# Kernel tuning notes

Hardware: AMD Instinct MI355X
Metric: run time of the kernel (lower is better)

Reference implementation:

```python
import jax, jax.numpy as jnp
import numpy as np

DN = ('NCHW', 'OIHW', 'NCHW')

def conv(x, w, b=None, pad='SAME'):
    y = jax.lax.conv_general_dilated(x, w, (1, 1), pad, dimension_numbers=DN)
    if b is not None:
        y = y + b[None, :, None, None]
    return y

def prelu(x, a):
    return jnp.where(x >= 0, x, a * x)

def ca_layer(x, w_a, w_b):
    # global avg pool -> 1x1 conv -> relu -> 1x1 conv -> sigmoid -> gate
    g = jnp.mean(x, axis=(2, 3), keepdims=True)          # [B,C,1,1]
    g = jax.nn.relu(conv(g, w_a))
    g = jax.nn.sigmoid(conv(g, w_b))
    return x * g

def head(x, w, b, ca_a, ca_b):
    y = conv(x, w, b)                                    # [B,4,H,W]
    y = ca_layer(y, ca_a, ca_b)
    return jax.nn.softmax(y, axis=1)                     # Softmax2d = softmax over C

def box_kernel(k):
    return jnp.full((1, 1, k, k), 1.0 / (k * k), dtype=jnp.float32)

def multiscale_blur(x):
    # SAME-padded uniform box filters of sizes 1,5,15,25 on [B,1,H,W]
    return [x if k == 1 else conv(x, box_kernel(k)) for k in (1, 5, 15, 25)]

def weighted_combine(h, blurs):
    # h: [B,4,H,W] softmax weights; blurs: list of 4 [B,1,H,W]
    return sum(h[:, i:i+1] * blurs[i] for i in range(4))

def setup_inputs() -> dict:
    key = jax.random.key(0)
    ks = jax.random.split(key, 32)
    B, H, W = 8, 512, 512
    s = 0.05
    inp = {
        'x':  jax.random.normal(ks[0], (B, 1, H, W), jnp.float32),
        'w1': jax.random.normal(ks[1], (32, 1, 3, 3), jnp.float32) * s,
        'b1': jnp.zeros((32,), jnp.float32),
        'a1': jnp.float32(0.25),
        'w2': jax.random.normal(ks[2], (64, 32, 3, 3), jnp.float32) * s,
        'b2': jnp.zeros((64,), jnp.float32),
        'a2': jnp.float32(0.25),
        'w3': jax.random.normal(ks[3], (32, 64, 3, 3), jnp.float32) * s,
        'b3': jnp.zeros((32,), jnp.float32),
        'a3': jnp.float32(0.25),
    }
    for i, kk in zip((1, 2, 3), (4, 8, 12)):
        inp[f'hw{i}'] = jax.random.normal(ks[kk], (4, 32, 3, 3), jnp.float32) * s
        inp[f'hb{i}'] = jnp.zeros((4,), jnp.float32)
        inp[f'ca{i}a'] = jax.random.normal(ks[kk + 1], (4, 4, 1, 1), jnp.float32) * s
        inp[f'ca{i}b'] = jax.random.normal(ks[kk + 2], (4, 4, 1, 1), jnp.float32) * s
    return inp

def reference(x, w1, b1, a1, w2, b2, a2, w3, b3, a3,
              hw1, hb1, ca1a, ca1b, hw2, hb2, ca2a, ca2b, hw3, hb3, ca3a, ca3b):
    body = prelu(conv(x, w1, b1), a1)
    body = prelu(conv(body, w2, b2), a2)
    body = prelu(conv(body, w3, b3), a3)            # [B,32,H,W]
    h1 = head(body, hw1, hb1, ca1a, ca1b)
    h2 = head(body, hw2, hb2, ca2a, ca2b)
    h3 = head(body, hw3, hb3, ca3a, ca3b)
    out1 = weighted_combine(h1, multiscale_blur(x))
    out2 = weighted_combine(h2, multiscale_blur(out1))
    out3 = weighted_combine(h3, multiscale_blur(out2))
    return out3
```

## Files before the change

kernel.cpp:

```cpp
#include <hip/hip_runtime.h>

#define HH 512
#define WW 512
#define NB 8
#define HWSZ (HH * WW)
#define PW 516
#define PROWS 514

typedef float f32x4 __attribute__((ext_vector_type(4)));
typedef float f32x16 __attribute__((ext_vector_type(16)));
typedef short bf16x8 __attribute__((ext_vector_type(8)));

__device__ __forceinline__ unsigned short f2bf(float f) {
  union { float f; unsigned u; } v; v.f = f;
  unsigned r = v.u + 0x7FFFu + ((v.u >> 16) & 1u);
  return (unsigned short)(r >> 16);
}
__device__ __forceinline__ float bf2f(unsigned u16) {
  union { unsigned u; float f; } v; v.u = u16 << 16;
  return v.f;
}

__device__ __forceinline__ void gload16(const uint4* g, uint4* l) {
  __builtin_amdgcn_global_load_lds((__attribute__((address_space(1))) void*)g,
                                   (__attribute__((address_space(3))) void*)l, 16, 0, 0);
}

#define PS1 ((size_t)PROWS * PW * 32)
#define PS2 ((size_t)PROWS * PW * 64)
#define NZ1 (2 * 4 * PW * 8 + 512 * 4 * 16)
#define NZ2 (2 * 8 * PW * 8 + 512 * 8 * 16)

__device__ __forceinline__ void zp(unsigned short* buf, int NCH, int i) {
  int rowShorts = NCH * PW * 8;
  if (i < 2 * rowShorts) {
    size_t r = (i < rowShorts) ? 0 : 513;
    int j = i % rowShorts;
    buf[r * rowShorts + j] = 0;
    return;
  }
  i -= 2 * rowShorts;
  int perRow = NCH * 16;
  int r = 1 + i / perRow;
  int j = i % perRow;
  int ch = j >> 4;
  int c = (j & 8) ? 513 : 0;
  int e = j & 7;
  buf[(((size_t)r * NCH + ch) * PW + c) * 8 + e] = 0;
}

__global__ __launch_bounds__(256) void k_prep(const float* __restrict__ w2,
                                              const float* __restrict__ w3,
                                              const float* __restrict__ h0,
                                              const float* __restrict__ h1,
                                              const float* __restrict__ h2,
                                              unsigned short* __restrict__ wp2,
                                              unsigned short* __restrict__ wp3,
                                              unsigned short* __restrict__ wph,
                                              unsigned short* __restrict__ t1,
                                              unsigned short* __restrict__ t2,
                                              float* __restrict__ S) {
  int i = blockIdx.x * 256 + threadIdx.x;
  const int N1 = 9 * 64 * 32;
  const int N2 = N1 + 9 * 32 * 64;
  const int N3 = N2 + 9 * 16 * 32;
  const int N4 = N3 + 4 * NZ1;
  const int N5 = N4 + 4 * NZ2;
  const int N6 = N5 + 128;
  if (i < N1) {
    int ic = i & 31, t = i >> 5, oc = t & 63, k = t >> 6;
    wp2[i] = f2bf(w2[(oc * 32 + ic) * 9 + k]);
  } else if (i < N2) {
    int j = i - N1;
    int ic = j & 63, t = j >> 6, oc = t & 31, k = t >> 5;
    wp3[j] = f2bf(w3[(oc * 64 + ic) * 9 + k]);
  } else if (i < N3) {
    int j = i - N2;
    int ic = j & 31, t = j >> 5, oc = t & 15, k = t >> 4;
    float v = 0.f;
    if (oc < 12) {
      const float* w = oc < 4 ? h0 : (oc < 8 ? h1 : h2);
      v = w[((oc & 3) * 32 + ic) * 9 + k];
    }
    wph[j] = f2bf(v);
  } else if (i < N4) {
    int j = i - N3;
    zp(t1 + (size_t)(j / NZ1) * PS1, 4, j % NZ1);
  } else if (i < N5) {
    int j = i - N4;
    zp(t2 + (size_t)(j / NZ2) * PS2, 8, j % NZ2);
  } else if (i < N6) {
    S[i - N5] = 0.f;
  }
}

__global__ __launch_bounds__(256) void k_conv1(const float* __restrict__ x,
                                               const float* __restrict__ w,
                                               const float* __restrict__ bias,
                                               const float* __restrict__ a_ptr,
                                               unsigned short* __restrict__ out) {
  const float* xp = x + (size_t)blockIdx.z * HWSZ;
  uint4* out4 = (uint4*)(out + (size_t)blockIdx.z * PS1);
  int pix = blockIdx.x * 256 + threadIdx.x;
  int h = pix >> 9, wc = pix & 511;
  float t[9];
#pragma unroll
  for (int dh = 0; dh < 3; dh++)
#pragma unroll
    for (int dw = 0; dw < 3; dw++) {
      int hh = h + dh - 1, ww = wc + dw - 1;
      t[dh * 3 + dw] =
          (hh >= 0 && hh < HH && ww >= 0 && ww < WW) ? xp[hh * WW + ww] : 0.f;
    }
  float a = a_ptr[0];
  unsigned pk[16];
#pragma unroll
  for (int oc = 0; oc < 32; oc++) {
    float s = bias[oc];
#pragma unroll
    for (int k = 0; k < 9; k++) s = fmaf(w[oc * 9 + k], t[k], s);
    s = s >= 0.f ? s : a * s;
    unsigned short b = f2bf(s);
    if (oc & 1)
      pk[oc >> 1] |= ((unsigned)b) << 16;
    else
      pk[oc >> 1] = b;
  }
#pragma unroll
  for (int q = 0; q < 4; q++)
    out4[((size_t)(h + 1) * 4 + q) * PW + (wc + 1)] = *(uint4*)&pk[q * 4];
}

__global__ __launch_bounds__(256, 2) void k_convm2(const unsigned short* __restrict__ in,
                                                   const unsigned short* __restrict__ wp,
                                                   const float* __restrict__ bias,
                                                   const float* __restrict__ a_ptr,
                                                   unsigned short* __restrict__ out) {
  __shared__ __align__(16) short ring[10 * 4 * 68 * 8];
  __shared__ __align__(16) short wlds[9 * 64 * 32];
  const int tid = threadIdx.x, lane = tid & 63, wid = tid >> 6;
  const int l31 = lane & 31, h16 = lane >> 5;
  const int c0 = blockIdx.x * 64;
  const int R0 = blockIdx.y * 32;
  const uint4* in4 = (const uint4*)(in + (size_t)blockIdx.z * PS1);
  unsigned short* outz = out + (size_t)blockIdx.z * PS2;
  uint4* ring4 = (uint4*)ring;
  uint4* wl4 = (uint4*)wlds;

  for (int c = tid; c < 9 * 64 * 4; c += 256) {
    int q = c & 3;
    int oc = (c >> 2) & 63;
    uint4 v = *(const uint4*)(wp + (size_t)(c >> 2) * 32 + q * 8);
    wl4[(c & ~3) | (q ^ (oc & 3))] = v;
  }

  auto load_rows = [&](int rfirst, int nrows) {
    int nseg = nrows * 4;
    for (int sg = wid; sg < nseg; sg += 4) {
      int rr = rfirst + (sg >> 2);
      int ch = sg & 3;
      const uint4* src = in4 + (size_t)(rr * 4 + ch) * PW + c0;
      uint4* dst = ring4 + ((rr % 10) * 4 + ch) * 68;
      gload16(src + lane, dst);
      gload16(src + 4 + lane, dst + 4);
    }
  };

  const float alpha = a_ptr[0];
  load_rows(R0, 6);

  for (int k = 0; k < 8; ++k) {
    const int rb = R0 + 4 * k;
    __syncthreads();
    if (k < 7) load_rows(rb + 6, 4);

    f32x16 acc[2][2];
#pragma unroll
    for (int nt = 0; nt < 2; nt++)
#pragma unroll
      for (int mt = 0; mt < 2; mt++)
#pragma unroll
        for (int j = 0; j < 16; j++) acc[nt][mt][j] = 0.f;

#pragma unroll
    for (int dh = 0; dh < 3; dh++) {
      bf16x8 af[3][2][2];
#pragma unroll
      for (int dw = 0; dw < 3; dw++)
#pragma unroll
        for (int ks = 0; ks < 2; ks++)
#pragma unroll
          for (int mt = 0; mt < 2; mt++)
            af[dw][ks][mt] = *(const bf16x8*)(
                wlds + ((((dh * 3 + dw) * 64 + mt * 32 + l31) * 4 +
                         ((ks * 2 + h16) ^ (l31 & 3))) * 8));
      const short* lrow = ring + (size_t)(((rb + wid + dh) % 10) * 4) * 68 * 8;
#pragma unroll
      for (int dw = 0; dw < 3; dw++) {
        const int pl0 = l31 + dw, pl1 = 32 + l31 + dw;
#pragma unroll
        for (int ks = 0; ks < 2; ks++) {
          const int blk = ks * 2 + h16;
          bf16x8 b0 = *(const bf16x8*)(lrow + (blk * 68 + pl0) * 8);
          bf16x8 b1 = *(const bf16x8*)(lrow + (blk * 68 + pl1) * 8);
#pragma unroll
          for (int mt = 0; mt < 2; mt++)
            acc[0][mt] = __builtin_amdgcn_mfma_f32_32x32x16_bf16(af[dw][ks][mt],
                                                                 b0, acc[0][mt], 0, 0, 0);
#pragma unroll
          for (int mt = 0; mt < 2; mt++)
            acc[1][mt] = __builtin_amdgcn_mfma_f32_32x32x16_bf16(af[dw][ks][mt],
                                                                 b1, acc[1][mt], 0, 0, 0);
        }
      }
    }

    const int orow = rb + wid + 1;
    uint2* o2 = (uint2*)outz;
#pragma unroll
    for (int nt = 0; nt < 2; nt++) {
      const int ocol = c0 + nt * 32 + l31 + 1;
#pragma unroll
      for (int mt = 0; mt < 2; mt++)
#pragma unroll
        for (int g = 0; g < 4; g++) {
          int oc0 = mt * 32 + g * 8 + h16 * 4;
          f32x4 bv = *(const f32x4*)(bias + oc0);
          float v[4];
#pragma unroll
          for (int j = 0; j < 4; j++) {
            float s = acc[nt][mt][g * 4 + j] + bv[j];
            v[j] = s >= 0.f ? s : alpha * s;
          }
          uint2 pk;
          pk.x = (unsigned)f2bf(v[0]) | ((unsigned)f2bf(v[1]) << 16);
          pk.y = (unsigned)f2bf(v[2]) | ((unsigned)f2bf(v[3]) << 16);
          size_t idx16 = ((size_t)orow * 8 + (mt * 4 + g)) * PW + ocol;
          o2[idx16 * 2 + h16] = pk;
        }
    }
  }
}

__global__ __launch_bounds__(256, 2) void k_convm3(const unsigned short* __restrict__ in,
                                                   const unsigned short* __restrict__ wp,
                                                   const float* __restrict__ bias,
                                                   const float* __restrict__ a_ptr,
                                                   unsigned short* __restrict__ out) {
  __shared__ __align__(16) short lds[8 * 8 * 68 * 8];
  const int tid = threadIdx.x, lane = tid & 63, wid = tid >> 6;
  const int l31 = lane & 31, h16 = lane >> 5;
  const int c0 = blockIdx.x * 64;
  const int R0 = blockIdx.y * 32;
  const uint4* in4 = (const uint4*)(in + (size_t)blockIdx.z * PS2);
  unsigned short* outz = out + (size_t)blockIdx.z * PS1;
  uint4* lds4 = (uint4*)lds;

  bf16x8 af[9][4];
#pragma unroll
  for (int k9 = 0; k9 < 9; k9++)
#pragma unroll
    for (int ks = 0; ks < 4; ks++)
      af[k9][ks] = *(const bf16x8*)(
          wp + ((size_t)(k9 * 32 + l31) * 64 + ks * 16 + h16 * 8));

  auto load_rows = [&](int rfirst, int nrows) {
    int nseg = nrows * 8;
    for (int sg = wid; sg < nseg; sg += 4) {
      int rr = rfirst + (sg >> 3);
      int ch = sg & 7;
      const uint4* src = in4 + (size_t)(rr * 8 + ch) * PW + c0;
      uint4* dst = lds4 + ((rr & 7) * 8 + ch) * 68;
      gload16(src + lane, dst);
      gload16(src + 4 + lane, dst + 4);
    }
  };

  const float alpha = a_ptr[0];
  load_rows(R0, 6);

  for (int k = 0; k < 8; ++k) {
    const int rb = R0 + 4 * k;
    __syncthreads();
    if (k < 7) load_rows(rb + 6, 2);

    f32x16 acc[2];
#pragma unroll
    for (int nt = 0; nt < 2; nt++)
#pragma unroll
      for (int j = 0; j < 16; j++) acc[nt][j] = 0.f;

#pragma unroll
    for (int dh = 0; dh < 3; dh++) {
      const short* lrow = lds + (size_t)(((rb + wid + dh) & 7) * 8) * 68 * 8;
#pragma unroll
      for (int dw = 0; dw < 3; dw++) {
        const int pl0 = l31 + dw, pl1 = 32 + l31 + dw;
#pragma unroll
        for (int ks = 0; ks < 4; ks++) {
          const int blk = ks * 2 + h16;
          bf16x8 b0 = *(const bf16x8*)(lrow + (blk * 68 + pl0) * 8);
          bf16x8 b1 = *(const bf16x8*)(lrow + (blk * 68 + pl1) * 8);
          acc[0] = __builtin_amdgcn_mfma_f32_32x32x16_bf16(af[dh * 3 + dw][ks],
                                                           b0, acc[0], 0, 0, 0);
          acc[1] = __builtin_amdgcn_mfma_f32_32x32x16_bf16(af[dh * 3 + dw][ks],
                                                           b1, acc[1], 0, 0, 0);
        }
      }
    }

    const int orow = rb + wid + 1;
    uint2* o2 = (uint2*)outz;
#pragma unroll
    for (int nt = 0; nt < 2; nt++) {
      const int ocol = c0 + nt * 32 + l31 + 1;
#pragma unroll
      for (int g = 0; g < 4; g++) {
        int oc0 = g * 8 + h16 * 4;
        f32x4 bv = *(const f32x4*)(bias + oc0);
        float v[4];
#pragma unroll
        for (int j = 0; j < 4; j++) {
          float s = acc[nt][g * 4 + j] + bv[j];
          v[j] = s >= 0.f ? s : alpha * s;
        }
        uint2 pk;
        pk.x = (unsigned)f2bf(v[0]) | ((unsigned)f2bf(v[1]) << 16);
        pk.y = (unsigned)f2bf(v[2]) | ((unsigned)f2bf(v[3]) << 16);
        size_t idx16 = ((size_t)orow * 4 + g) * PW + ocol;
        o2[idx16 * 2 + h16] = pk;
      }
    }
    __syncthreads();
    if (k < 7) load_rows(rb + 8, 2);
  }
}

__global__ __launch_bounds__(256) void k_headm(const unsigned short* __restrict__ in,
                                               const unsigned short* __restrict__ wp,
                                               const float* __restrict__ hb0,
                                               const float* __restrict__ hb1,
                                               const float* __restrict__ hb2,
                                               unsigned short* __restrict__ pre,
                                               float* __restrict__ S) {
  __shared__ __align__(16) short lds[4 * 132 * 32];
  const int tid = threadIdx.x;
  const int r0 = blockIdx.y * 2, c0 = blockIdx.x * 128;
  const uint4* in4 = (const uint4*)(in + (size_t)blockIdx.z * PS1);
  float* Sz = S + blockIdx.z * 16;
  uint4* lds4 = (uint4*)lds;
  for (int i = tid; i < 4 * 4 * 130; i += 256) {
    int pcol = i % 130;
    int t = i / 130;
    int ch = t & 3;
    int prow = t >> 2;
    uint4 v = in4[(size_t)((r0 + prow) * 4 + ch) * PW + (c0 + pcol)];
    int pl = prow * 132 + pcol;
    lds4[pl * 4 + (ch ^ ((pl >> 1) & 3))] = v;
  }
  __syncthreads();

  const int lane = tid & 63, wid = tid >> 6;
  const int l15 = lane & 15, q = lane >> 4;
  const int rowsel = wid >> 1, half = wid & 1;

  f32x4 acc[4];
#pragma unroll
  for (int i = 0; i < 4; i++)
#pragma unroll
    for (int j = 0; j < 4; j++) acc[i][j] = 0.f;

#pragma unroll
  for (int dh = 0; dh < 3; dh++) {
    bf16x8 af[3];
#pragma unroll
    for (int dw = 0; dw < 3; dw++)
      af[dw] = *(const bf16x8*)(wp + ((dh * 3 + dw) * 16 + l15) * 32 + q * 8);
    const int lrow = (rowsel + dh) * 132;
#pragma unroll
    for (int dw = 0; dw < 3; dw++) {
#pragma unroll
      for (int nt = 0; nt < 4; nt++) {
        int pl = lrow + half * 64 + nt * 16 + l15 + dw;
        int blk = q ^ ((pl >> 1) & 3);
        bf16x8 b = *(const bf16x8*)(&lds[(pl * 4 + blk) * 8]);
        acc[nt] = __builtin_amdgcn_mfma_f32_16x16x32_bf16(af[dw], b, acc[nt], 0, 0, 0);
      }
    }
  }

  float bs[4];
#pragma unroll
  for (int r = 0; r < 4; r++) {
    int oc = q * 4 + r;
    bs[r] = oc < 4 ? hb0[oc] : (oc < 8 ? hb1[oc - 4] : (oc < 12 ? hb2[oc - 8] : 0.f));
  }
  unsigned short* prehq = pre + ((size_t)(q * 4 + blockIdx.z) * HWSZ) * 4;
  float csum[4] = {0.f, 0.f, 0.f, 0.f};
  const int orow = r0 + rowsel;
#pragma unroll
  for (int nt = 0; nt < 4; nt++) {
    int pcol = c0 + half * 64 + nt * 16 + l15;
    int pix = orow * 512 + pcol;
    float v[4];
#pragma unroll
    for (int r = 0; r < 4; r++) {
      v[r] = acc[nt][r] + bs[r];
      csum[r] += v[r];
    }
    uint2 pk;
    pk.x = (unsigned)f2bf(v[0]) | ((unsigned)f2bf(v[1]) << 16);
    pk.y = (unsigned)f2bf(v[2]) | ((unsigned)f2bf(v[3]) << 16);
    *(uint2*)(prehq + (size_t)pix * 4) = pk;
  }
#pragma unroll
  for (int d = 1; d < 16; d <<= 1)
#pragma unroll
    for (int r = 0; r < 4; r++) csum[r] += __shfl_xor(csum[r], d, 64);
  __shared__ float part[4][4][4];
  if (l15 == 0)
#pragma unroll
    for (int r = 0; r < 4; r++) part[wid][q][r] = csum[r];
  __syncthreads();
  if (tid < 12) {
    int oc = tid;
    float s = part[0][oc >> 2][oc & 3] + part[1][oc >> 2][oc & 3] +
              part[2][oc >> 2][oc & 3] + part[3][oc >> 2][oc & 3];
    atomicAdd(&Sz[oc], s);
  }
}

#define BT 32
#define RAD 12
#define SRCT (BT + 2 * RAD)
__global__ __launch_bounds__(256) void k_blurcombine(const float* __restrict__ src,
                                                     const unsigned short* __restrict__ preh,
                                                     const float* __restrict__ S4,
                                                     const float* __restrict__ wa,
                                                     const float* __restrict__ wb,
                                                     float* __restrict__ dst) {
  __shared__ float tile[SRCT][SRCT];
  __shared__ float hs[3][SRCT][BT];
  __shared__ float g[4];
  const float* srcz = src + (size_t)blockIdx.z * HWSZ;
  const unsigned short* prez = preh + (size_t)blockIdx.z * HWSZ * 4;
  const float* S4z = S4 + blockIdx.z * 16;
  float* dstz = dst + (size_t)blockIdx.z * HWSZ;
  int h0 = blockIdx.y * BT - RAD, w0 = blockIdx.x * BT - RAD;
  if (threadIdx.x < 4) {
    int o = threadIdx.x;
    float m[4], ga[4];
#pragma unroll
    for (int c = 0; c < 4; c++) m[c] = S4z[c] * (1.0f / (float)HWSZ);
#pragma unroll
    for (int c = 0; c < 4; c++) {
      float s = 0.f;
#pragma unroll
      for (int j = 0; j < 4; j++) s = fmaf(wa[c * 4 + j], m[j], s);
      ga[c] = fmaxf(s, 0.f);
    }
    float s2 = 0.f;
#pragma unroll
    for (int c = 0; c < 4; c++) s2 = fmaf(wb[o * 4 + c], ga[c], s2);
    g[o] = 1.f / (1.f + expf(-s2));
  }
  for (int idx = threadIdx.x; idx < SRCT * SRCT; idx += 256) {
    int r = idx / SRCT, c = idx % SRCT;
    int hh = h0 + r, ww = w0 + c;
    float v = 0.f;
    if (hh >= 0 && hh < HH && ww >= 0 && ww < WW) v = srcz[hh * WW + ww];
    tile[r][c] = v;
  }
  __syncthreads();
  for (int idx = threadIdx.x; idx < SRCT * BT; idx += 256) {
    int r = idx / BT, j = idx % BT;
    int cc = j + RAD;
    float s5 = 0.f;
#pragma unroll
    for (int d = -2; d <= 2; d++) s5 += tile[r][cc + d];
    float s15 = s5;
#pragma unroll
    for (int d = 3; d <= 7; d++) s15 += tile[r][cc + d] + tile[r][cc - d];
    float s25 = s15;
#pragma unroll
    for (int d = 8; d <= 12; d++) s25 += tile[r][cc + d] + tile[r][cc - d];
    hs[0][r][j] = s5;
    hs[1][r][j] = s15;
    hs[2][r][j] = s25;
  }
  __syncthreads();
  for (int p = threadIdx.x; p < BT * BT; p += 256) {
    int i = p / BT, j = p % BT;
    int rr = i + RAD;
    float b1 = 0.f;
#pragma unroll
    for (int d = -2; d <= 2; d++) b1 += hs[0][rr + d][j];
    float b2 = 0.f;
#pragma unroll
    for (int d = -7; d <= 7; d++) b2 += hs[1][rr + d][j];
    float b3 = 0.f;
#pragma unroll
    for (int d = -12; d <= 12; d++) b3 += hs[2][rr + d][j];
    b1 *= (1.f / 25.f);
    b2 *= (1.f / 225.f);
    b3 *= (1.f / 625.f);
    float b0 = tile[rr][j + RAD];
    int y = blockIdx.y * BT + i, x = blockIdx.x * BT + j;
    int pix = y * WW + x;
    uint2 pk = *(const uint2*)(prez + (size_t)pix * 4);
    float v[4];
    v[0] = bf2f(pk.x & 0xffffu) * g[0];
    v[1] = bf2f(pk.x >> 16) * g[1];
    v[2] = bf2f(pk.y & 0xffffu) * g[2];
    v[3] = bf2f(pk.y >> 16) * g[3];
    float mx = fmaxf(fmaxf(v[0], v[1]), fmaxf(v[2], v[3]));
    float e0 = expf(v[0] - mx), e1 = expf(v[1] - mx), e2 = expf(v[2] - mx),
          e3 = expf(v[3] - mx);
    float inv = 1.f / (e0 + e1 + e2 + e3);
    dstz[pix] = (e0 * b0 + e1 * b1 + e2 * b2 + e3 * b3) * inv;
  }
}

extern "C" void kernel_launch(void* const* d_in, const int* in_sizes, int n_in,
                              void* d_out, int out_size, void* d_ws, size_t ws_size,
                              hipStream_t stream) {
  const float* x = (const float*)d_in[0];
  const float* w1 = (const float*)d_in[1];
  const float* b1 = (const float*)d_in[2];
  const float* a1 = (const float*)d_in[3];
  const float* w2 = (const float*)d_in[4];
  const float* b2 = (const float*)d_in[5];
  const float* a2 = (const float*)d_in[6];
  const float* w3 = (const float*)d_in[7];
  const float* b3 = (const float*)d_in[8];
  const float* a3 = (const float*)d_in[9];
  const float* hw[3] = {(const float*)d_in[10], (const float*)d_in[14], (const float*)d_in[18]};
  const float* hb[3] = {(const float*)d_in[11], (const float*)d_in[15], (const float*)d_in[19]};
  const float* caa[3] = {(const float*)d_in[12], (const float*)d_in[16], (const float*)d_in[20]};
  const float* cab[3] = {(const float*)d_in[13], (const float*)d_in[17], (const float*)d_in[21]};

  char* base = (char*)d_ws;
  size_t off = 0;
  auto alloc = [&](size_t bytes) {
    char* p = base + off;
    off = (off + bytes + 63) & ~(size_t)63;
    return p;
  };
  unsigned short* t1 = (unsigned short*)alloc(4 * PS1 * 2);
  unsigned short* t2 = (unsigned short*)alloc(4 * PS2 * 2);
  unsigned short* pre = (unsigned short*)alloc(16 * (size_t)HWSZ * 4 * 2);
  unsigned short* wp2 = (unsigned short*)alloc(9 * 64 * 32 * 2);
  unsigned short* wp3 = (unsigned short*)alloc(9 * 64 * 32 * 2);
  unsigned short* wph = (unsigned short*)alloc(9 * 16 * 32 * 2);
  float* out1 = (float*)alloc(4 * (size_t)HWSZ * 4);
  float* out2 = (float*)alloc(4 * (size_t)HWSZ * 4);
  float* S = (float*)alloc(8 * 16 * 4);

  dim3 blk(256);
  {
    int total = 9 * 64 * 32 + 9 * 32 * 64 + 9 * 16 * 32 + 4 * NZ1 + 4 * NZ2 + 128;
    k_prep<<<(total + 255) / 256, blk, 0, stream>>>(w2, w3, hw[0], hw[1], hw[2], wp2,
                                                    wp3, wph, t1, t2, S);
  }

  dim3 gc1(1024, 1, 4);
  dim3 gconv(8, 16, 4);
  dim3 ghead(4, 256, 4);
  dim3 gbc(WW / BT, HH / BT, 4);
  const size_t preplane = (size_t)HWSZ * 4;
  for (int g = 0; g < 2; g++) {
    const float* xg = x + (size_t)g * 4 * HWSZ;
    float* Sg = S + g * 64;
    float* outg = (float*)d_out + (size_t)g * 4 * HWSZ;
    k_conv1<<<gc1, blk, 0, stream>>>(xg, w1, b1, a1, t1);
    k_convm2<<<gconv, blk, 0, stream>>>(t1, wp2, b2, a2, t2);
    k_convm3<<<gconv, blk, 0, stream>>>(t2, wp3, b3, a3, t1);
    k_headm<<<ghead, blk, 0, stream>>>(t1, wph, hb[0], hb[1], hb[2], pre, Sg);
    k_blurcombine<<<gbc, blk, 0, stream>>>(xg, pre + 0 * 4 * preplane, Sg + 0, caa[0], cab[0], out1);
    k_blurcombine<<<gbc, blk, 0, stream>>>(out1, pre + 1 * 4 * preplane, Sg + 4, caa[1], cab[1], out2);
    k_blurcombine<<<gbc, blk, 0, stream>>>(out2, pre + 2 * 4 * preplane, Sg + 8, caa[2], cab[2], outg);
  }
}
```

Measured before the change: 551.0 us.

## Restructure head conv as persistent row-streaming tiles with async LDS ring

Rewrites the head conv kernel so each block owns a 64-column by 32-row strip. Input rows stream through an 8-row LDS ring buffer using async global-to-LDS loads, and the next two rows are prefetched while the current four are computed. Weight fragments are loaded into registers once per block, and the grid shrinks from 4096 tiny blocks to 512. The aim is to cut the redundant halo reloads and per-block setup of the old 2-row tiles and to overlap loads with MFMA work, at the cost of fewer, longer blocks and lower parallelism.

After: 480.0 us. -12.9%, faster.

```diff
diff --git a/kernel.cpp b/kernel.cpp
--- a/kernel.cpp
+++ b/kernel.cpp
@@ -336,58 +336,27 @@
   }
 }
 
-__global__ __launch_bounds__(256) void k_headm(const unsigned short* __restrict__ in,
-                                               const unsigned short* __restrict__ wp,
-                                               const float* __restrict__ hb0,
-                                               const float* __restrict__ hb1,
-                                               const float* __restrict__ hb2,
-                                               unsigned short* __restrict__ pre,
-                                               float* __restrict__ S) {
-  __shared__ __align__(16) short lds[4 * 132 * 32];
-  const int tid = threadIdx.x;
-  const int r0 = blockIdx.y * 2, c0 = blockIdx.x * 128;
+__global__ __launch_bounds__(256, 2) void k_headm(const unsigned short* __restrict__ in,
+                                                  const unsigned short* __restrict__ wp,
+                                                  const float* __restrict__ hb0,
+                                                  const float* __restrict__ hb1,
+                                                  const float* __restrict__ hb2,
+                                                  unsigned short* __restrict__ pre,
+                                                  float* __restrict__ S) {
+  __shared__ __align__(16) short lds[8 * 4 * 68 * 8];
+  __shared__ float part[4][4][4];
+  const int tid = threadIdx.x, lane = tid & 63, wid = tid >> 6;
+  const int l15 = lane & 15, q = lane >> 4;
+  const int c0 = blockIdx.x * 64;
+  const int R0 = blockIdx.y * 32;
   const uint4* in4 = (const uint4*)(in + (size_t)blockIdx.z * PS1);
   float* Sz = S + blockIdx.z * 16;
   uint4* lds4 = (uint4*)lds;
-  for (int i = tid; i < 4 * 4 * 130; i += 256) {
-    int pcol = i % 130;
-    int t = i / 130;
-    int ch = t & 3;
-    int prow = t >> 2;
-    uint4 v = in4[(size_t)((r0 + prow) * 4 + ch) * PW + (c0 + pcol)];
-    int pl = prow * 132 + pcol;
-    lds4[pl * 4 + (ch ^ ((pl >> 1) & 3))] = v;
-  }
-  __syncthreads();
-
-  const int lane = tid & 63, wid = tid >> 6;
-  const int l15 = lane & 15, q = lane >> 4;
-  const int rowsel = wid >> 1, half = wid & 1;
-
-  f32x4 acc[4];
-#pragma unroll
-  for (int i = 0; i < 4; i++)
-#pragma unroll
-    for (int j = 0; j < 4; j++) acc[i][j] = 0.f;
-
-#pragma unroll
-  for (int dh = 0; dh < 3; dh++) {
-    bf16x8 af[3];
-#pragma unroll
-    for (int dw = 0; dw < 3; dw++)
-      af[dw] = *(const bf16x8*)(wp + ((dh * 3 + dw) * 16 + l15) * 32 + q * 8);
-    const int lrow = (rowsel + dh) * 132;
-#pragma unroll
-    for (int dw = 0; dw < 3; dw++) {
-#pragma unroll
-      for (int nt = 0; nt < 4; nt++) {
-        int pl = lrow + half * 64 + nt * 16 + l15 + dw;
-        int blk = q ^ ((pl >> 1) & 3);
-        bf16x8 b = *(const bf16x8*)(&lds[(pl * 4 + blk) * 8]);
-        acc[nt] = __builtin_amdgcn_mfma_f32_16x16x32_bf16(af[dw], b, acc[nt], 0, 0, 0);
-      }
-    }
-  }
+
+  bf16x8 af[9];
+#pragma unroll
+  for (int k9 = 0; k9 < 9; k9++)
+    af[k9] = *(const bf16x8*)(wp + (size_t)(k9 * 16 + l15) * 32 + q * 8);
 
   float bs[4];
 #pragma unroll
@@ -396,28 +365,71 @@
     bs[r] = oc < 4 ? hb0[oc] : (oc < 8 ? hb1[oc - 4] : (oc < 12 ? hb2[oc - 8] : 0.f));
   }
   unsigned short* prehq = pre + ((size_t)(q * 4 + blockIdx.z) * HWSZ) * 4;
+
+  auto load_rows = [&](int rfirst, int nrows) {
+    int nseg = nrows * 4;
+    for (int sg = wid; sg < nseg; sg += 4) {
+      int rr = rfirst + (sg >> 2);
+      int ch = sg & 3;
+      const uint4* src = in4 + (size_t)(rr * 4 + ch) * PW + c0;
+      uint4* dst = lds4 + ((rr & 7) * 4 + ch) * 68;
+      gload16(src + lane, dst);
+      gload16(src + 4 + lane, dst + 4);
+    }
+  };
+
+  load_rows(R0, 6);
   float csum[4] = {0.f, 0.f, 0.f, 0.f};
-  const int orow = r0 + rowsel;
-#pragma unroll
-  for (int nt = 0; nt < 4; nt++) {
-    int pcol = c0 + half * 64 + nt * 16 + l15;
-    int pix = orow * 512 + pcol;
-    float v[4];
-#pragma unroll
-    for (int r = 0; r < 4; r++) {
-      v[r] = acc[nt][r] + bs[r];
-      csum[r] += v[r];
-    }
-    uint2 pk;
-    pk.x = (unsigned)f2bf(v[0]) | ((unsigned)f2bf(v[1]) << 16);
-    pk.y = (unsigned)f2bf(v[2]) | ((unsigned)f2bf(v[3]) << 16);
-    *(uint2*)(prehq + (size_t)pix * 4) = pk;
-  }
+
+  for (int k = 0; k < 8; ++k) {
+    const int rb = R0 + 4 * k;
+    __syncthreads();
+    if (k < 7) load_rows(rb + 6, 2);
+
+    f32x4 acc[4];
+#pragma unroll
+    for (int nt = 0; nt < 4; nt++)
+#pragma unroll
+      for (int j = 0; j < 4; j++) acc[nt][j] = 0.f;
+
+#pragma unroll
+    for (int dh = 0; dh < 3; dh++) {
+      const short* lrow = lds + (size_t)(((rb + wid + dh) & 7) * 4) * 68 * 8;
+#pragma unroll
+      for (int dw = 0; dw < 3; dw++) {
+        bf16x8 a = af[dh * 3 + dw];
+#pragma unroll
+        for (int nt = 0; nt < 4; nt++) {
+          int pl = nt * 16 + l15 + dw;
+          bf16x8 b = *(const bf16x8*)(lrow + (q * 68 + pl) * 8);
+          acc[nt] = __builtin_amdgcn_mfma_f32_16x16x32_bf16(a, b, acc[nt], 0, 0, 0);
+        }
+      }
+    }
+
+    const int orow = rb + wid;
+#pragma unroll
+    for (int nt = 0; nt < 4; nt++) {
+      int pix = orow * 512 + c0 + nt * 16 + l15;
+      float v[4];
+#pragma unroll
+      for (int r = 0; r < 4; r++) {
+        v[r] = acc[nt][r] + bs[r];
+        csum[r] += v[r];
+      }
+      uint2 pk;
+      pk.x = (unsigned)f2bf(v[0]) | ((unsigned)f2bf(v[1]) << 16);
+      pk.y = (unsigned)f2bf(v[2]) | ((unsigned)f2bf(v[3]) << 16);
+      *(uint2*)(prehq + (size_t)pix * 4) = pk;
+    }
+    __syncthreads();
+    if (k < 7) load_rows(rb + 8, 2);
+  }
+
 #pragma unroll
   for (int d = 1; d < 16; d <<= 1)
 #pragma unroll
     for (int r = 0; r < 4; r++) csum[r] += __shfl_xor(csum[r], d, 64);
-  __shared__ float part[4][4][4];
   if (l15 == 0)
 #pragma unroll
     for (int r = 0; r < 4; r++) part[wid][q][r] = csum[r];
@@ -565,7 +577,6 @@
 
   dim3 gc1(1024, 1, 4);
   dim3 gconv(8, 16, 4);
-  dim3 ghead(4, 256, 4);
   dim3 gbc(WW / BT, HH / BT, 4);
   const size_t preplane = (size_t)HWSZ * 4;
   for (int g = 0; g < 2; g++) {
@@ -575,7 +586,7 @@
     k_conv1<<<gc1, blk, 0, stream>>>(xg, w1, b1, a1, t1);
     k_convm2<<<gconv, blk, 0, stream>>>(t1, wp2, b2, a2, t2);
     k_convm3<<<gconv, blk, 0, stream>>>(t2, wp3, b3, a3, t1);
-    k_headm<<<ghead, blk, 0, stream>>>(t1, wph, hb[0], hb[1], hb[2], pre, Sg);
+    k_headm<<<gconv, blk, 0, stream>>>(t1, wph, hb[0], hb[1], hb[2], pre, Sg);
     k_blurcombine<<<gbc, blk, 0, stream>>>(xg, pre + 0 * 4 * preplane, Sg + 0, caa[0], cab[0], out1);
     k_blurcombine<<<gbc, blk, 0, stream>>>(out1, pre + 1 * 4 * preplane, Sg + 4, caa[1], cab[1], out2);
     k_blurcombine<<<gbc, blk, 0, stream>>>(out2, pre + 2 * 4 * preplane, Sg + 8, caa[2], cab[2], outg);
```
